# Optimization experiments

Hardware: AMD Instinct MI355X
Metric: run time of the kernel (lower is better)

Reference implementation:

```python
import jax, jax.numpy as jnp
from jax import lax
import numpy as np

B, C, T = 4, 4, 4096
H, INNER, S, L = 256, 512, 64, 3
V, MAXPOS = 1024, 20000
DILS = (1, 3, 6, 12)


def setup_inputs():
    key = jax.random.key(0)
    ks = iter(jax.random.split(key, 32))
    f = lambda *sh: jax.random.normal(next(ks), sh, jnp.float32) * 0.02
    return {
        "audio_tokens": jax.random.randint(next(ks), (B, C, T), 0, V),
        "text_context": jax.random.normal(next(ks), (B, H), jnp.float32),
        "tok_emb": f(C, V, H),
        "pos_emb": f(MAXPOS, H),
        "in_w": f(L, 2 * INNER, H),
        "conv_w": f(L, INNER, 1, 4),
        "conv_b": f(L, INNER),
        "D": jnp.zeros((L, INNER), jnp.float32),
        "Bp_w": f(L, S, INNER),
        "Cp_w": f(L, INNER, S),
        "out_w": f(L, H, INNER),
        "ln_g": jnp.ones((L, H), jnp.float32),
        "ln_b": jnp.zeros((L, H), jnp.float32),
        "pat_w": f(4, H // 4, H, 3),
        "pat_b": f(4, H // 4),
        "fus_w": f(H, 2 * H),
        "fus_b": jnp.zeros((H,), jnp.float32),
        "fus_g": jnp.ones((H,), jnp.float32),
        "fus_bb": jnp.zeros((H,), jnp.float32),
        "head_w": f(C, V, H),
        "head_b": jnp.zeros((C, V), jnp.float32),
        "position_offset": 0,
    }


def _ln(x, g, b, eps=1e-5):
    m = jnp.mean(x, -1, keepdims=True)
    v = jnp.mean(jnp.square(x - m), -1, keepdims=True)
    return (x - m) * lax.rsqrt(v + eps) * g + b


def _mamba(x, in_w, conv_w, conv_b, Dp, Bp_w, Cp_w, out_w, g, b):
    Bb = x.shape[0]
    xp = x @ in_w.T                              # [B,T,2*INNER]
    xi, xg = xp[..., :INNER], xp[..., INNER:]
    # depthwise causal conv (torch pad=3 both sides then [:T] == left-pad 3)
    xc = lax.conv_general_dilated(
        xi.transpose(0, 2, 1), conv_w, (1,), [(3, 0)],
        feature_group_count=INNER,
        dimension_numbers=("NCH", "OIH", "NCH")) + conv_b[None, :, None]
    xc = jax.nn.silu(xc.transpose(0, 2, 1))      # [B,T,INNER]
    u = xc @ Bp_w.T                              # [B,T,S]

    def step(h, ut):
        h = 0.95 * h + 0.05 * ut
        return h, h

    _, hs = lax.scan(step, jnp.zeros((Bb, S), x.dtype), u.transpose(1, 0, 2))
    y = hs.transpose(1, 0, 2) @ Cp_w.T + Dp * xc
    y = (y * jax.nn.silu(xg)) @ out_w.T
    return _ln(y + x, g, b)


def _forward(audio_tokens, text_context, tok_emb, pos_emb, in_w, conv_w, conv_b,
             D, Bp_w, Cp_w, out_w, ln_g, ln_b, pat_w, pat_b, fus_w, fus_b,
             fus_g, fus_bb, head_w, head_b, position_offset):
    # per-codebook embedding, mean over codebooks -> [B,T,H]
    emb = jnp.mean(tok_emb[jnp.arange(C)[None, :, None], audio_tokens], axis=1)
    pos = pos_emb[position_offset + jnp.arange(T)]
    audio_emb = emb + pos[None] + text_context[:, None, :]
    feat = audio_emb
    for i in range(L):
        feat = _mamba(feat, in_w[i], conv_w[i], conv_b[i], D[i],
                      Bp_w[i], Cp_w[i], out_w[i], ln_g[i], ln_b[i])
    ac = audio_emb.transpose(0, 2, 1)            # [B,H,T]
    pats = []
    for i, d in enumerate(DILS):
        p = lax.conv_general_dilated(ac, pat_w[i], (1,), [(d, d)],
                                     rhs_dilation=(d,),
                                     dimension_numbers=("NCH", "OIH", "NCH"))
        pats.append(p + pat_b[i][None, :, None])
    pat = jnp.concatenate(pats, 1).transpose(0, 2, 1)   # [B,T,H]
    comb = jnp.concatenate([feat, pat], -1)              # [B,T,2H]
    fused = _ln(jax.nn.relu(comb @ fus_w.T + fus_b), fus_g, fus_bb)
    logits = jnp.einsum("bth,cvh->bctv", fused, head_w) + head_b[None, :, None, :]
    return logits                                        # [B,C,T,V]


def reference(audio_tokens, text_context, tok_emb, pos_emb, in_w, conv_w, conv_b,
              D, Bp_w, Cp_w, out_w, ln_g, ln_b, pat_w, pat_b, fus_w, fus_b,
              fus_g, fus_bb, head_w, head_b, position_offset):
    return _forward(audio_tokens, text_context, tok_emb, pos_emb, in_w, conv_w,
                    conv_b, D, Bp_w, Cp_w, out_w, ln_g, ln_b, pat_w, pat_b,
                    fus_w, fus_b, fus_g, fus_bb, head_w, head_b, position_offset)
```

## Files before the change

### kernel.cpp

```cpp
#include <hip/hip_runtime.h>

#define B_ 4
#define C_ 4
#define T_ 4096
#define H_ 256
#define INNER_ 512
#define S_ 64
#define L_ 3
#define V_ 1024
#define NTOK (B_*T_)
#define TPAD (T_+24)

typedef __attribute__((ext_vector_type(8))) short short8v;
typedef __attribute__((ext_vector_type(4))) float f32x4;

__device__ __forceinline__ float siluf(float x) { return x / (1.0f + expf(-x)); }

__device__ __forceinline__ unsigned short f2bf(float x) {
    unsigned u = __float_as_uint(x);
    u = (u + 0x7FFFu + ((u >> 16) & 1u)) >> 16;
    return (unsigned short)u;
}
__device__ __forceinline__ float bf2f(unsigned short v) {
    return __uint_as_float(((unsigned)v) << 16);
}

template<int BN>
__global__ __launch_bounds__(256) void gemm_mfma(
    const unsigned short* __restrict__ Ag, int lda,
    const unsigned short* __restrict__ Bg, int ldb,
    float* __restrict__ Cg, int ldc,
    int K, int flags, const float* __restrict__ bias,
    int bstride, int roff, int patmode)
{
    constexpr int FM  = (BN == 128) ? 4 : 2;
    constexpr int FN  = 4;
    constexpr int BCH = (BN == 128) ? 2 : 1;
    __shared__ __attribute__((aligned(16))) unsigned short Alds[128 * 32];
    __shared__ __attribute__((aligned(16))) unsigned short Blds[BN * 32];

    int tid = threadIdx.x;
    int wid = tid >> 6, lane = tid & 63;
    int qq = lane >> 4, l16 = lane & 15;
    int wm, wn;
    if (BN == 128) { wm = wid >> 1; wn = wid & 1; } else { wm = wid; wn = 0; }

    int n0 = blockIdx.x * 128;
    int m0; const unsigned short* Bp; float* Cb; int ro = roff;
    if (patmode) {
        int g = blockIdx.y;
        int d = (g == 0) ? 1 : (g == 1) ? 3 : (g == 2) ? 6 : 12;
        ro = 12 + ((patmode == 1) ? -d : d);
        m0 = 0;
        Bp = Bg + (size_t)((g << 1) + (patmode - 1)) * (64 * 256);
        Cb = Cg + g * 64;
    } else {
        m0 = blockIdx.y * BN; Bp = Bg; Cb = Cg;
    }
    const unsigned short* Ab = Ag +
        (size_t)(bstride ? ((n0 >> 12) * bstride + (n0 & (T_ - 1)) + ro) : n0) * lda;

    f32x4 acc[FM][FN] = {};

    for (int k0 = 0; k0 < K; k0 += 32) {
        short8v av[2], bv[BCH];
#pragma unroll
        for (int it = 0; it < 2; ++it) {
            int u = tid + (it << 8);
            int row = u >> 2, cb = u & 3;
            av[it] = *(const short8v*)(Ab + (size_t)row * lda + k0 + cb * 8);
        }
#pragma unroll
        for (int it = 0; it < BCH; ++it) {
            int u = tid + (it << 8);
            int row = u >> 2, cb = u & 3;
            bv[it] = *(const short8v*)(Bp + (size_t)(m0 + row) * ldb + k0 + cb * 8);
        }
        __syncthreads();
#pragma unroll
        for (int it = 0; it < 2; ++it) {
            int u = tid + (it << 8);
            int row = u >> 2, cb = u & 3;
            *(short8v*)(Alds + (row >> 4) * 512 + cb * 128 + (row & 15) * 8) = av[it];
        }
#pragma unroll
        for (int it = 0; it < BCH; ++it) {
            int u = tid + (it << 8);
            int row = u >> 2, cb = u & 3;
            *(short8v*)(Blds + (row >> 4) * 512 + cb * 128 + (row & 15) * 8) = bv[it];
        }
        __syncthreads();
        short8v afr[FM], bfr[FN];
#pragma unroll
        for (int i = 0; i < FM; ++i)
            afr[i] = *(const short8v*)(Alds + (wm * FM + i) * 512 + lane * 8);
#pragma unroll
        for (int j = 0; j < FN; ++j)
            bfr[j] = *(const short8v*)(Blds + (wn * FN + j) * 512 + lane * 8);
#pragma unroll
        for (int i = 0; i < FM; ++i)
#pragma unroll
            for (int j = 0; j < FN; ++j)
                acc[i][j] = __builtin_amdgcn_mfma_f32_16x16x32_bf16(afr[i], bfr[j], acc[i][j], 0, 0, 0);
    }

#pragma unroll
    for (int i = 0; i < FM; ++i) {
#pragma unroll
        for (int r = 0; r < 4; ++r) {
            int row = n0 + wm * (FM * 16) + i * 16 + qq * 4 + r;
#pragma unroll
            for (int j = 0; j < FN; ++j) {
                int col = m0 + wn * (FN * 16) + j * 16 + l16;
                float v = acc[i][j][r];
                if (bias) v += bias[col];
                if (flags & 4) {
                    int bb2 = row >> 12, t = row & (T_ - 1);
                    int cc = col >> 10, vv = col & (V_ - 1);
                    Cg[((size_t)(((bb2 << 2) + cc) << 12) + t) * V_ + vv] = v;
                } else if (flags & 2) {
                    ((unsigned short*)Cb)[(size_t)row * ldc + col] = f2bf(v);
                } else if (flags & 1) {
                    float* p = Cb + (size_t)row * ldc + col;
                    *p = *p + v;
                } else {
                    Cb[(size_t)row * ldc + col] = v;
                }
            }
        }
    }
}

__global__ __launch_bounds__(256) void k_embed(
    const int* __restrict__ tok, const float* __restrict__ text,
    const float* __restrict__ tok_emb, const float* __restrict__ pos_emb,
    const int* __restrict__ pos_off, float* __restrict__ A, unsigned short* __restrict__ Apad)
{
    int gid = blockIdx.x * 256 + threadIdx.x;
    int h = gid & (H_ - 1);
    int n = gid >> 8;
    int b = n >> 12, t = n & (T_ - 1);
    float acc = 0.f;
#pragma unroll
    for (int c = 0; c < C_; ++c) {
        int tk = tok[((b * C_ + c) << 12) + t];
        acc += tok_emb[(c * V_ + tk) * H_ + h];
    }
    int po = pos_off[0];
    acc = acc * 0.25f + pos_emb[(po + t) * H_ + h] + text[b * H_ + h];
    A[(size_t)n * H_ + h] = acc;
    Apad[((size_t)b * TPAD + 12 + t) * H_ + h] = f2bf(acc);
}

__global__ void k_zeropad(unsigned short* __restrict__ Apad)
{
    int blk = blockIdx.x;
    int b = blk / 24, rw = blk % 24;
    int rr = rw < 12 ? rw : T_ + rw;
    Apad[((size_t)b * TPAD + rr) * H_ + threadIdx.x] = 0;
}

__global__ __launch_bounds__(256) void k_wconv(
    const float* __restrict__ inw, const float* __restrict__ outw,
    const float* __restrict__ bpw, const float* __restrict__ fusw,
    const float* __restrict__ headw,
    unsigned short* __restrict__ dinw, unsigned short* __restrict__ doutw,
    unsigned short* __restrict__ dbpw, unsigned short* __restrict__ dfusw,
    unsigned short* __restrict__ dheadw)
{
    int i = blockIdx.x * 256 + threadIdx.x;
    if (i < 786432)        dinw[i] = f2bf(inw[i]);
    else if (i < 1179648)  doutw[i - 786432]  = f2bf(outw[i - 786432]);
    else if (i < 1277952)  dbpw[i - 1179648]  = f2bf(bpw[i - 1179648]);
    else if (i < 1409024)  dfusw[i - 1277952] = f2bf(fusw[i - 1277952]);
    else                   dheadw[i - 1409024] = f2bf(headw[i - 1409024]);
}

__global__ __launch_bounds__(256) void k_pack_pat(
    const float* __restrict__ pw, unsigned short* __restrict__ w0,
    unsigned short* __restrict__ wk)
{
    int idx = blockIdx.x * 256 + threadIdx.x;
    if (idx < 65536) {
        int oc = idx >> 8, cin = idx & 255;
        w0[idx] = f2bf(pw[(oc * 256 + cin) * 3 + 1]);
    } else {
        int j = idx - 65536;
        int g = j >> 14, o = (j >> 8) & 63, cin = j & 255;
        int id = g >> 1, kk = (g & 1) * 2;
        wk[j] = f2bf(pw[((id * 64 + o) * 256 + cin) * 3 + kk]);
    }
}

__global__ __launch_bounds__(256) void k_conv(
    const unsigned short* __restrict__ XPb, const float* __restrict__ cw,
    const float* __restrict__ cb, unsigned short* __restrict__ XCb)
{
    int gid = blockIdx.x * 256 + threadIdx.x;
    int i = gid & (INNER_ - 1);
    int n = gid >> 9;
    int b = n >> 12, t = n & (T_ - 1);
    float acc = cb[i];
#pragma unroll
    for (int k = 0; k < 4; ++k) {
        int tt = t - 3 + k;
        if (tt >= 0) acc += bf2f(XPb[(size_t)((b << 12) + tt) * 1024 + i]) * cw[i * 4 + k];
    }
    XCb[(size_t)n * INNER_ + i] = f2bf(siluf(acc));
}

__global__ void k_scan_local(float* __restrict__ U, float* __restrict__ hend)
{
    int blk = blockIdx.x;
    int b = blk >> 6, c = blk & 63;
    int s = threadIdx.x;
    float* p = U + ((size_t)(b << 12) + c * 64) * 64 + s;
    float h = 0.f;
#pragma unroll 4
    for (int t = 0; t < 64; ++t) { h = 0.95f * h + 0.05f * p[t * 64]; p[t * 64] = h; }
    hend[(size_t)blk * 64 + s] = h;
}

__global__ void k_scan_apply(float* __restrict__ U, const float* __restrict__ hend)
{
    int blk = blockIdx.x;
    int b = blk >> 6, c = blk & 63;
    int s = threadIdx.x;
    if (c == 0) return;
    const float F = 0.03752414f;
    float Hc = 0.f;
    for (int cc = 0; cc < c; ++cc) Hc = hend[(size_t)((b << 6) + cc) * 64 + s] + F * Hc;
    float* p = U + ((size_t)(b << 12) + c * 64) * 64 + s;
    float w = 0.95f;
#pragma unroll 4
    for (int t = 0; t < 64; ++t) { p[t * 64] += w * Hc; w *= 0.95f; }
}

__global__ __launch_bounds__(256) void k_ymix(
    const float* __restrict__ HS, const float* __restrict__ Cp,
    const float* __restrict__ Dp, unsigned short* __restrict__ XCb,
    const unsigned short* __restrict__ XPb)
{
    const int NB = 4;
    int n0 = blockIdx.x * NB;
    __shared__ float hsL[NB * 64];
    int tid = threadIdx.x;
    {
        int nn = tid >> 6, s = tid & 63;
        hsL[tid] = HS[(size_t)(n0 + nn) * 64 + s];
    }
    __syncthreads();
#pragma unroll
    for (int half = 0; half < 2; ++half) {
        int i = tid + half * 256;
        float acc[NB] = {};
        const float* cp = Cp + i * 64;
        for (int s = 0; s < 64; ++s) {
            float w = cp[s];
#pragma unroll
            for (int nn = 0; nn < NB; ++nn) acc[nn] += hsL[nn * 64 + s] * w;
        }
        float d = Dp[i];
#pragma unroll
        for (int nn = 0; nn < NB; ++nn) {
            size_t n = n0 + nn;
            float xc = bf2f(XCb[n * INNER_ + i]);
            float xg = bf2f(XPb[n * 1024 + 512 + i]);
            XCb[n * INNER_ + i] = f2bf((acc[nn] + d * xc) * siluf(xg));
        }
    }
}

__global__ __launch_bounds__(256) void k_ln(
    const float* __restrict__ Yo, const float* __restrict__ Xin,
    const float* __restrict__ g, const float* __restrict__ bb,
    float* __restrict__ Out, unsigned short* __restrict__ Obf, int obfld)
{
    int n = blockIdx.x, h = threadIdx.x;
    float x = Yo[(size_t)n * H_ + h] + Xin[(size_t)n * H_ + h];
    float s = x, sq = x * x;
#pragma unroll
    for (int off = 32; off >= 1; off >>= 1) {
        s  += __shfl_down(s, off, 64);
        sq += __shfl_down(sq, off, 64);
    }
    __shared__ float rs[4], rq[4];
    int wid = h >> 6, lane = h & 63;
    if (lane == 0) { rs[wid] = s; rq[wid] = sq; }
    __syncthreads();
    float S = rs[0] + rs[1] + rs[2] + rs[3];
    float Q = rq[0] + rq[1] + rq[2] + rq[3];
    float m = S * (1.f / H_);
    float v = fmaxf(Q * (1.f / H_) - m * m, 0.f);
    float r = rsqrtf(v + 1e-5f);
    float y = (x - m) * r * g[h] + bb[h];
    Out[(size_t)n * H_ + h] = y;
    Obf[(size_t)n * obfld + h] = f2bf(y);
}

__global__ __launch_bounds__(256) void k_fusln(
    const float* __restrict__ Pre, const float* __restrict__ fb,
    const float* __restrict__ fg, const float* __restrict__ fbb,
    unsigned short* __restrict__ Outb)
{
    int n = blockIdx.x, h = threadIdx.x;
    float x = fmaxf(Pre[(size_t)n * H_ + h] + fb[h], 0.f);
    float s = x, sq = x * x;
#pragma unroll
    for (int off = 32; off >= 1; off >>= 1) {
        s  += __shfl_down(s, off, 64);
        sq += __shfl_down(sq, off, 64);
    }
    __shared__ float rs[4], rq[4];
    int wid = h >> 6, lane = h & 63;
    if (lane == 0) { rs[wid] = s; rq[wid] = sq; }
    __syncthreads();
    float S = rs[0] + rs[1] + rs[2] + rs[3];
    float Q = rq[0] + rq[1] + rq[2] + rq[3];
    float m = S * (1.f / H_);
    float v = fmaxf(Q * (1.f / H_) - m * m, 0.f);
    float r = rsqrtf(v + 1e-5f);
    Outb[(size_t)n * H_ + h] = f2bf((x - m) * r * fg[h] + fbb[h]);
}

__global__ __launch_bounds__(256) void k_pat2comb(
    const float* __restrict__ PAT, unsigned short* __restrict__ COMB)
{
    int i = blockIdx.x * 256 + threadIdx.x;
    int n = i >> 8, h = i & 255;
    COMB[(size_t)n * 512 + 256 + h] = f2bf(PAT[i]);
}

extern "C" void kernel_launch(void* const* d_in, const int* in_sizes, int n_in,
                              void* d_out, int out_size, void* d_ws, size_t ws_size,
                              hipStream_t stream)
{
    (void)in_sizes; (void)n_in; (void)out_size; (void)ws_size;
    const int*   tok      = (const int*)d_in[0];
    const float* text     = (const float*)d_in[1];
    const float* tok_emb  = (const float*)d_in[2];
    const float* pos_emb  = (const float*)d_in[3];
    const float* in_w     = (const float*)d_in[4];
    const float* conv_w   = (const float*)d_in[5];
    const float* conv_b   = (const float*)d_in[6];
    const float* Dw       = (const float*)d_in[7];
    const float* Bp_w     = (const float*)d_in[8];
    const float* Cp_w     = (const float*)d_in[9];
    const float* out_w    = (const float*)d_in[10];
    const float* ln_g     = (const float*)d_in[11];
    const float* ln_b     = (const float*)d_in[12];
    const float* pat_w    = (const float*)d_in[13];
    const float* pat_b    = (const float*)d_in[14];
    const float* fus_w    = (const float*)d_in[15];
    const float* fus_b    = (const float*)d_in[16];
    const float* fus_g    = (const float*)d_in[17];
    const float* fus_bb   = (const float*)d_in[18];
    const float* head_w   = (const float*)d_in[19];
    const float* head_b   = (const float*)d_in[20];
    const int*   pos_off  = (const int*)d_in[21];

    float* W = (float*)d_ws;
    float* Abuf = W;
    float* F0   = W + 4194304;
    float* F1   = W + 8388608;
    float* U    = W + 12582912;
    float* HEND = W + 13631488;
    unsigned short* XPbf = (unsigned short*)(W + 13647872);
    unsigned short* XCbf = (unsigned short*)(W + 22036480);
    unsigned short* Fbf  = (unsigned short*)(W + 26230784);
    unsigned short* COMB = (unsigned short*)(W + 28327936);
    unsigned short* Apad = (unsigned short*)(W + 32522240);
    float* PATF = W + 13647872;
    float* FUSP = W + 13647872 + 4194304;
    unsigned short* inwb   = (unsigned short*)(W + 34631680);
    unsigned short* outwb  = (unsigned short*)(W + 35024896);
    unsigned short* bpwb   = (unsigned short*)(W + 35221504);
    unsigned short* fuswb  = (unsigned short*)(W + 35270656);
    unsigned short* headwb = (unsigned short*)(W + 35336192);
    unsigned short* w0b    = (unsigned short*)(W + 35860480);
    unsigned short* wkb    = (unsigned short*)(W + 35893248);

    k_embed<<<NTOK * H_ / 256, 256, 0, stream>>>(tok, text, tok_emb, pos_emb, pos_off, Abuf, Apad);
    k_zeropad<<<96, 256, 0, stream>>>(Apad);
    k_wconv<<<9600, 256, 0, stream>>>(in_w, out_w, Bp_w, fus_w, head_w,
                                      inwb, outwb, bpwb, fuswb, headwb);
    k_pack_pat<<<768, 256, 0, stream>>>(pat_w, w0b, wkb);

    const float* fin = Abuf;
    float* fouts[3] = {F0, F1, F0};
    for (int l = 0; l < L_; ++l) {
        const unsigned short* Ain = (l == 0) ? Apad : Fbf;
        gemm_mfma<128><<<dim3(128, 8), 256, 0, stream>>>(
            Ain, H_, inwb + (size_t)l * 262144, H_, (float*)XPbf, 1024,
            H_, 2, nullptr, (l == 0) ? TPAD : 0, 12, 0);
        k_conv<<<NTOK * INNER_ / 256, 256, 0, stream>>>(
            XPbf, conv_w + l * INNER_ * 4, conv_b + l * INNER_, XCbf);
        gemm_mfma<64><<<dim3(128, 1), 256, 0, stream>>>(
            XCbf, INNER_, bpwb + (size_t)l * S_ * INNER_, INNER_, U, S_,
            INNER_, 0, nullptr, 0, 0, 0);
        k_scan_local<<<256, 64, 0, stream>>>(U, HEND);
        k_scan_apply<<<256, 64, 0, stream>>>(U, HEND);
        k_ymix<<<NTOK / 4, 256, 0, stream>>>(
            U, Cp_w + l * INNER_ * S_, Dw + l * INNER_, XCbf, XPbf);
        gemm_mfma<128><<<dim3(128, 2), 256, 0, stream>>>(
            XCbf, INNER_, outwb + (size_t)l * H_ * INNER_, INNER_, fouts[l], H_,
            INNER_, 0, nullptr, 0, 0, 0);
        k_ln<<<NTOK, 256, 0, stream>>>(fouts[l], fin, ln_g + l * H_, ln_b + l * H_,
                                       fouts[l], (l == 2) ? COMB : Fbf, (l == 2) ? 512 : 256);
        fin = fouts[l];
    }

    gemm_mfma<128><<<dim3(128, 2), 256, 0, stream>>>(
        Apad, H_, w0b, H_, PATF, H_, H_, 0, pat_b, TPAD, 12, 0);
    gemm_mfma<64><<<dim3(128, 4), 256, 0, stream>>>(
        Apad, H_, wkb, H_, PATF, H_, H_, 1, nullptr, TPAD, 12, 1);
    gemm_mfma<64><<<dim3(128, 4), 256, 0, stream>>>(
        Apad, H_, wkb, H_, PATF, H_, H_, 1, nullptr, TPAD, 12, 2);
    k_pat2comb<<<16384, 256, 0, stream>>>(PATF, COMB);

    gemm_mfma<128><<<dim3(128, 2), 256, 0, stream>>>(
        COMB, 512, fuswb, 512, FUSP, H_, 512, 0, nullptr, 0, 0, 0);
    k_fusln<<<NTOK, 256, 0, stream>>>(FUSP, fus_b, fus_g, fus_bb, Fbf);

    gemm_mfma<128><<<dim3(128, 32), 256, 0, stream>>>(
        Fbf, H_, headwb, H_, (float*)d_out, V_, H_, 4, head_b, 0, 0, 0);
}
```

Before: 1.306 ms.

## Double-buffer GEMM LDS, fuse pattern conv taps into one GEMM, vectorize conv

The GEMM kernel now double-buffers its LDS tiles so the global loads for the next K-slice overlap the MFMA work on the current one. The three dilated-conv pattern GEMMs (centre tap plus two side taps) and the separate fp32-to-bf16 copy kernel become one GEMM launch. It loops over the three taps, accumulates in registers and writes bf16 straight into the COMB buffer, removing the fp32 read-modify-write and an extra pass. The depthwise conv kernel processes four channels per thread with vector loads and stores. Costs are twice the LDS per block, which may lower occupancy, and more complex tap indexing.

```diff
diff --git a/kernel.cpp b/kernel.cpp
--- a/kernel.cpp
+++ b/kernel.cpp
@@ -12,6 +12,7 @@
 #define TPAD (T_+24)
 
 typedef __attribute__((ext_vector_type(8))) short short8v;
+typedef __attribute__((ext_vector_type(4))) short short4v;
 typedef __attribute__((ext_vector_type(4))) float f32x4;
 
 __device__ __forceinline__ float siluf(float x) { return x / (1.0f + expf(-x)); }
@@ -36,8 +37,8 @@
     constexpr int FM  = (BN == 128) ? 4 : 2;
     constexpr int FN  = 4;
     constexpr int BCH = (BN == 128) ? 2 : 1;
-    __shared__ __attribute__((aligned(16))) unsigned short Alds[128 * 32];
-    __shared__ __attribute__((aligned(16))) unsigned short Blds[BN * 32];
+    __shared__ __attribute__((aligned(16))) unsigned short Alds[2][128 * 32];
+    __shared__ __attribute__((aligned(16))) unsigned short Blds[2][BN * 32];
 
     int tid = threadIdx.x;
     int wid = tid >> 6, lane = tid & 63;
@@ -46,62 +47,96 @@
     if (BN == 128) { wm = wid >> 1; wn = wid & 1; } else { wm = wid; wn = 0; }
 
     int n0 = blockIdx.x * 128;
-    int m0; const unsigned short* Bp; float* Cb; int ro = roff;
-    if (patmode) {
-        int g = blockIdx.y;
-        int d = (g == 0) ? 1 : (g == 1) ? 3 : (g == 2) ? 6 : 12;
-        ro = 12 + ((patmode == 1) ? -d : d);
-        m0 = 0;
-        Bp = Bg + (size_t)((g << 1) + (patmode - 1)) * (64 * 256);
-        Cb = Cg + g * 64;
-    } else {
-        m0 = blockIdx.y * BN; Bp = Bg; Cb = Cg;
-    }
-    const unsigned short* Ab = Ag +
-        (size_t)(bstride ? ((n0 >> 12) * bstride + (n0 & (T_ - 1)) + ro) : n0) * lda;
+    int g = blockIdx.y;
+    int arow = tid >> 2, acb = tid & 3;
+
+    int m0 = (patmode == 3) ? 0 : g * BN;
+    float* Cb = (patmode == 3) ? (float*)((unsigned short*)Cg + 256 + g * 64) : Cg;
+    const float* biasp = (patmode == 3 && bias) ? bias + g * 64 : bias;
+    int d = (g == 0) ? 1 : (g == 1) ? 3 : (g == 2) ? 6 : 12;
 
     f32x4 acc[FM][FN] = {};
-
-    for (int k0 = 0; k0 < K; k0 += 32) {
-        short8v av[2], bv[BCH];
-#pragma unroll
-        for (int it = 0; it < 2; ++it) {
-            int u = tid + (it << 8);
-            int row = u >> 2, cb = u & 3;
-            av[it] = *(const short8v*)(Ab + (size_t)row * lda + k0 + cb * 8);
-        }
-#pragma unroll
-        for (int it = 0; it < BCH; ++it) {
-            int u = tid + (it << 8);
-            int row = u >> 2, cb = u & 3;
-            bv[it] = *(const short8v*)(Bp + (size_t)(m0 + row) * ldb + k0 + cb * 8);
-        }
+    int ntap = (patmode == 3) ? 3 : 1;
+
+    for (int tap = 0; tap < ntap; ++tap) {
+        const unsigned short* Bp;
+        int ro;
+        if (patmode == 3) {
+            ro = 12 + (tap == 0 ? -d : (tap == 2 ? d : 0));
+            Bp = (tap == 1) ? Bg + (size_t)g * (64 * 256)
+                            : Bg + 65536 + (size_t)((g << 1) + (tap >> 1)) * (64 * 256);
+        } else { ro = roff; Bp = Bg; }
+        const unsigned short* Ab = Ag +
+            (size_t)(bstride ? ((n0 >> 12) * bstride + (n0 & (T_ - 1)) + ro) : n0) * lda;
+
+        short8v pa0, pa1, pb0, pb1;
+        pa0 = *(const short8v*)(Ab + (size_t)arow * lda + acb * 8);
+        pa1 = *(const short8v*)(Ab + (size_t)(arow + 64) * lda + acb * 8);
+        pb0 = *(const short8v*)(Bp + (size_t)(m0 + arow) * ldb + acb * 8);
+        if (BCH == 2)
+            pb1 = *(const short8v*)(Bp + (size_t)(m0 + arow + 64) * ldb + acb * 8);
         __syncthreads();
-#pragma unroll
-        for (int it = 0; it < 2; ++it) {
-            int u = tid + (it << 8);
-            int row = u >> 2, cb = u & 3;
-            *(short8v*)(Alds + (row >> 4) * 512 + cb * 128 + (row & 15) * 8) = av[it];
-        }
-#pragma unroll
-        for (int it = 0; it < BCH; ++it) {
-            int u = tid + (it << 8);
-            int row = u >> 2, cb = u & 3;
-            *(short8v*)(Blds + (row >> 4) * 512 + cb * 128 + (row & 15) * 8) = bv[it];
+        {
+            int f0 = (arow >> 4) * 512 + acb * 128 + (arow & 15) * 8;
+            int r2 = arow + 64;
+            int f1 = (r2 >> 4) * 512 + acb * 128 + (r2 & 15) * 8;
+            *(short8v*)(&Alds[0][f0]) = pa0;
+            *(short8v*)(&Alds[0][f1]) = pa1;
+            *(short8v*)(&Blds[0][f0]) = pb0;
+            if (BCH == 2) *(short8v*)(&Blds[0][f1]) = pb1;
         }
         __syncthreads();
-        short8v afr[FM], bfr[FN];
-#pragma unroll
-        for (int i = 0; i < FM; ++i)
-            afr[i] = *(const short8v*)(Alds + (wm * FM + i) * 512 + lane * 8);
-#pragma unroll
-        for (int j = 0; j < FN; ++j)
-            bfr[j] = *(const short8v*)(Blds + (wn * FN + j) * 512 + lane * 8);
-#pragma unroll
-        for (int i = 0; i < FM; ++i)
+
+        int cur = 0;
+        for (int k0 = 32; k0 < K; k0 += 32) {
+            short8v na0, na1, nb0, nb1;
+            na0 = *(const short8v*)(Ab + (size_t)arow * lda + k0 + acb * 8);
+            na1 = *(const short8v*)(Ab + (size_t)(arow + 64) * lda + k0 + acb * 8);
+            nb0 = *(const short8v*)(Bp + (size_t)(m0 + arow) * ldb + k0 + acb * 8);
+            if (BCH == 2)
+                nb1 = *(const short8v*)(Bp + (size_t)(m0 + arow + 64) * ldb + k0 + acb * 8);
+
+            {
+                short8v afr[FM], bfr[FN];
+#pragma unroll
+                for (int i = 0; i < FM; ++i)
+                    afr[i] = *(const short8v*)(&Alds[cur][(wm * FM + i) * 512 + lane * 8]);
+#pragma unroll
+                for (int j = 0; j < FN; ++j)
+                    bfr[j] = *(const short8v*)(&Blds[cur][(wn * FN + j) * 512 + lane * 8]);
+#pragma unroll
+                for (int i = 0; i < FM; ++i)
+#pragma unroll
+                    for (int j = 0; j < FN; ++j)
+                        acc[i][j] = __builtin_amdgcn_mfma_f32_16x16x32_bf16(afr[i], bfr[j], acc[i][j], 0, 0, 0);
+            }
+
+            {
+                int f0 = (arow >> 4) * 512 + acb * 128 + (arow & 15) * 8;
+                int r2 = arow + 64;
+                int f1 = (r2 >> 4) * 512 + acb * 128 + (r2 & 15) * 8;
+                *(short8v*)(&Alds[cur ^ 1][f0]) = na0;
+                *(short8v*)(&Alds[cur ^ 1][f1]) = na1;
+                *(short8v*)(&Blds[cur ^ 1][f0]) = nb0;
+                if (BCH == 2) *(short8v*)(&Blds[cur ^ 1][f1]) = nb1;
+            }
+            __syncthreads();
+            cur ^= 1;
+        }
+        {
+            short8v afr[FM], bfr[FN];
+#pragma unroll
+            for (int i = 0; i < FM; ++i)
+                afr[i] = *(const short8v*)(&Alds[cur][(wm * FM + i) * 512 + lane * 8]);
 #pragma unroll
             for (int j = 0; j < FN; ++j)
-                acc[i][j] = __builtin_amdgcn_mfma_f32_16x16x32_bf16(afr[i], bfr[j], acc[i][j], 0, 0, 0);
+                bfr[j] = *(const short8v*)(&Blds[cur][(wn * FN + j) * 512 + lane * 8]);
+#pragma unroll
+            for (int i = 0; i < FM; ++i)
+#pragma unroll
+                for (int j = 0; j < FN; ++j)
+                    acc[i][j] = __builtin_amdgcn_mfma_f32_16x16x32_bf16(afr[i], bfr[j], acc[i][j], 0, 0, 0);
+        }
     }
 
 #pragma unroll
@@ -113,16 +148,13 @@
             for (int j = 0; j < FN; ++j) {
                 int col = m0 + wn * (FN * 16) + j * 16 + l16;
                 float v = acc[i][j][r];
-                if (bias) v += bias[col];
+                if (biasp) v += biasp[col];
                 if (flags & 4) {
                     int bb2 = row >> 12, t = row & (T_ - 1);
                     int cc = col >> 10, vv = col & (V_ - 1);
                     Cg[((size_t)(((bb2 << 2) + cc) << 12) + t) * V_ + vv] = v;
                 } else if (flags & 2) {
                     ((unsigned short*)Cb)[(size_t)row * ldc + col] = f2bf(v);
-                } else if (flags & 1) {
-                    float* p = Cb + (size_t)row * ldc + col;
-                    *p = *p + v;
                 } else {
                     Cb[(size_t)row * ldc + col] = v;
                 }
@@ -197,16 +229,26 @@
     const float* __restrict__ cb, unsigned short* __restrict__ XCb)
 {
     int gid = blockIdx.x * 256 + threadIdx.x;
-    int i = gid & (INNER_ - 1);
-    int n = gid >> 9;
+    int i4 = (gid & 127) << 2;
+    int n = gid >> 7;
     int b = n >> 12, t = n & (T_ - 1);
-    float acc = cb[i];
+    float acc[4];
+#pragma unroll
+    for (int j = 0; j < 4; ++j) acc[j] = cb[i4 + j];
 #pragma unroll
     for (int k = 0; k < 4; ++k) {
         int tt = t - 3 + k;
-        if (tt >= 0) acc += bf2f(XPb[(size_t)((b << 12) + tt) * 1024 + i]) * cw[i * 4 + k];
-    }
-    XCb[(size_t)n * INNER_ + i] = f2bf(siluf(acc));
+        if (tt >= 0) {
+            short4v v = *(const short4v*)(XPb + (size_t)((b << 12) + tt) * 1024 + i4);
+#pragma unroll
+            for (int j = 0; j < 4; ++j)
+                acc[j] += bf2f((unsigned short)v[j]) * cw[(i4 + j) * 4 + k];
+        }
+    }
+    short4v o;
+#pragma unroll
+    for (int j = 0; j < 4; ++j) o[j] = (short)f2bf(siluf(acc[j]));
+    *(short4v*)(XCb + (size_t)n * INNER_ + i4) = o;
 }
 
 __global__ void k_scan_local(float* __restrict__ U, float* __restrict__ hend)
@@ -321,14 +363,6 @@
     float v = fmaxf(Q * (1.f / H_) - m * m, 0.f);
     float r = rsqrtf(v + 1e-5f);
     Outb[(size_t)n * H_ + h] = f2bf((x - m) * r * fg[h] + fbb[h]);
-}
-
-__global__ __launch_bounds__(256) void k_pat2comb(
-    const float* __restrict__ PAT, unsigned short* __restrict__ COMB)
-{
-    int i = blockIdx.x * 256 + threadIdx.x;
-    int n = i >> 8, h = i & 255;
-    COMB[(size_t)n * 512 + 256 + h] = f2bf(PAT[i]);
 }
 
 extern "C" void kernel_launch(void* const* d_in, const int* in_sizes, int n_in,
@@ -370,8 +404,7 @@
     unsigned short* Fbf  = (unsigned short*)(W + 26230784);
     unsigned short* COMB = (unsigned short*)(W + 28327936);
     unsigned short* Apad = (unsigned short*)(W + 32522240);
-    float* PATF = W + 13647872;
-    float* FUSP = W + 13647872 + 4194304;
+    float* FUSP = W + 13647872;
     unsigned short* inwb   = (unsigned short*)(W + 34631680);
     unsigned short* outwb  = (unsigned short*)(W + 35024896);
     unsigned short* bpwb   = (unsigned short*)(W + 35221504);
@@ -393,7 +426,7 @@
         gemm_mfma<128><<<dim3(128, 8), 256, 0, stream>>>(
             Ain, H_, inwb + (size_t)l * 262144, H_, (float*)XPbf, 1024,
             H_, 2, nullptr, (l == 0) ? TPAD : 0, 12, 0);
-        k_conv<<<NTOK * INNER_ / 256, 256, 0, stream>>>(
+        k_conv<<<NTOK * 128 / 256, 256, 0, stream>>>(
             XPbf, conv_w + l * INNER_ * 4, conv_b + l * INNER_, XCbf);
         gemm_mfma<64><<<dim3(128, 1), 256, 0, stream>>>(
             XCbf, INNER_, bpwb + (size_t)l * S_ * INNER_, INNER_, U, S_,
@@ -410,13 +443,8 @@
         fin = fouts[l];
     }
 
-    gemm_mfma<128><<<dim3(128, 2), 256, 0, stream>>>(
-        Apad, H_, w0b, H_, PATF, H_, H_, 0, pat_b, TPAD, 12, 0);
     gemm_mfma<64><<<dim3(128, 4), 256, 0, stream>>>(
-        Apad, H_, wkb, H_, PATF, H_, H_, 1, nullptr, TPAD, 12, 1);
-    gemm_mfma<64><<<dim3(128, 4), 256, 0, stream>>>(
-        Apad, H_, wkb, H_, PATF, H_, H_, 1, nullptr, TPAD, 12, 2);
-    k_pat2comb<<<16384, 256, 0, stream>>>(PATF, COMB);
+        Apad, H_, w0b, H_, (float*)COMB, 512, H_, 2, pat_b, TPAD, 12, 3);
 
     gemm_mfma<128><<<dim3(128, 2), 256, 0, stream>>>(
         COMB, 512, fuswb, 512, FUSP, H_, 512, 0, nullptr, 0, 0, 0);
```

Result: no change. 1.285 ms (-1.6%).
